# Performance work log

Hardware: AMD Instinct MI355X
Metric: run time of the kernel (lower is better)

Reference implementation:

```python
import jax, jax.numpy as jnp
import numpy as np
from jax import lax

N_USERS, N_ITEMS = 40000, 60000
N = N_USERS + N_ITEMS
D = 64
E = 800000
L = 2
BIAS = 1e-4
AUTO_T = 1.0


def setup_inputs() -> dict:
    key = jax.random.key(0)
    ks = jax.random.split(key, 12)
    emb0 = jax.random.normal(ks[0], (N, D), dtype=jnp.float32) * 0.1
    h_idx = jax.random.randint(ks[1], (E,), 0, N)
    t_idx = jax.random.randint(ks[2], (E,), 0, N)
    # symmetric normalization G = D^-1/2 A D^-1/2 (values share A's sparsity)
    deg = jax.ops.segment_sum(jnp.ones((E,), jnp.float32), h_idx, num_segments=N)
    dis = jnp.where(deg > 0, deg ** -0.5, 0.0)
    G_values = dis[h_idx] * dis[t_idx]
    # Gumbel noise: -log(-log(U(bias, 1-bias)))
    ue = jax.random.uniform(ks[3], (L, E), minval=BIAS, maxval=1.0 - BIAS)
    edge_gumbel = -jnp.log(-jnp.log(ue))
    un = jax.random.uniform(ks[4], (L, N, D), minval=BIAS, maxval=1.0 - BIAS)
    emb_gumbel = -jnp.log(-jnp.log(un))
    sc2, sc1 = (2.0 / (3 * D)) ** 0.5, (2.0 / (2 * D)) ** 0.5
    edge_W1 = jax.random.normal(ks[5], (L, 2 * D, D), dtype=jnp.float32) * sc2
    edge_b1 = jnp.zeros((L, D), jnp.float32)
    edge_W2 = jax.random.normal(ks[6], (L, D, 1), dtype=jnp.float32) * sc1
    edge_b2 = jnp.zeros((L, 1), jnp.float32)
    emb_W1 = jax.random.normal(ks[7], (L, D, D), dtype=jnp.float32) * sc1
    emb_b1 = jnp.zeros((L, D), jnp.float32)
    emb_W2 = jax.random.normal(ks[8], (L, D, D), dtype=jnp.float32) * sc1
    emb_b2 = jnp.zeros((L, D), jnp.float32)
    return dict(emb0=emb0, h_idx=h_idx, t_idx=t_idx, G_values=G_values,
                edge_gumbel=edge_gumbel, emb_gumbel=emb_gumbel,
                edge_W1=edge_W1, edge_b1=edge_b1, edge_W2=edge_W2, edge_b2=edge_b2,
                emb_W1=emb_W1, emb_b1=emb_b1, emb_W2=emb_W2, emb_b2=emb_b2)


def _spmm(vals, h, t, x, n):
    # out[h] += vals * x[t]
    return jax.ops.segment_sum(vals[:, None] * x[t], h, num_segments=n)


def reference(emb0, h_idx, t_idx, G_values, edge_gumbel, emb_gumbel,
              edge_W1, edge_b1, edge_W2, edge_b2,
              emb_W1, emb_b1, emb_W2, emb_b2):
    n = emb0.shape[0]
    e0 = e1 = e2 = emb0
    s0 = s1 = s2 = emb0
    for i in range(edge_W1.shape[0]):
        # branch 0: plain normalized propagation
        gnn0 = _spmm(G_values, h_idx, t_idx, e0, n)
        # branch 1: learned edge reweighting (auto_augment_s, is_norm=True)
        edge_emb = jnp.concatenate([e1[h_idx], e1[t_idx]], axis=1)      # [E, 2D]
        logits = jnp.maximum(edge_emb @ edge_W1[i] + edge_b1[i], 0.0) @ edge_W2[i] + edge_b2[i]  # [E,1]
        w = jax.nn.sigmoid((edge_gumbel[i][:, None] + logits) / AUTO_T)[:, 0]
        w = lax.stop_gradient(w)                                         # detached in original
        row = jax.ops.segment_sum(w, h_idx, num_segments=n)
        dinv = jnp.where(row > 0, 1.0 / row, 0.0)                        # pow(-1).nan_to_num(0)
        vals1 = dinv[h_idx] * w
        gnn1 = _spmm(vals1, h_idx, t_idx, e1, n)
        # branch 2: learned feature gating (auto_augment_f)
        lg = jnp.maximum(e2 @ emb_W1[i] + emb_b1[i], 0.0) @ emb_W2[i] + emb_b2[i]
        gate = lax.stop_gradient(jax.nn.sigmoid((emb_gumbel[i] + lg) / AUTO_T))
        gnn2 = _spmm(G_values, h_idx, t_idx, gate * e2, n)
        e0 = gnn0 + e0
        e1 = gnn1 + e1
        e2 = gnn2 + e2
        s0 = s0 + e0
        s1 = s1 + e1
        s2 = s2 + e2
    return jnp.stack([s0, s1, s2])  # [3, N, D]; split rows into users/items downstream
```

## Files before the change

kernel.cpp:

```cpp
#include <hip/hip_runtime.h>
#include <hip/hip_bf16.h>
#include <math.h>

#define PK_STRIDE 256
#define LDA 72

typedef float v4f __attribute__((ext_vector_type(4)));
typedef __attribute__((ext_vector_type(8))) short s8;
typedef __attribute__((ext_vector_type(4))) float f4;

__device__ __forceinline__ float4 f4z() { return make_float4(0.f, 0.f, 0.f, 0.f); }
__device__ __forceinline__ void fma4(float4& a, float s, const float4& v) {
  a.x = fmaf(s, v.x, a.x); a.y = fmaf(s, v.y, a.y);
  a.z = fmaf(s, v.z, a.z); a.w = fmaf(s, v.w, a.w);
}
__device__ __forceinline__ float4 add4(const float4& a, const float4& b) {
  return make_float4(a.x + b.x, a.y + b.y, a.z + b.z, a.w + b.w);
}
__device__ __forceinline__ void stnt4(float* p, const float4& v) {
  v4f u; u.x = v.x; u.y = v.y; u.z = v.z; u.w = v.w;
  __builtin_nontemporal_store(u, (v4f*)p);
}
__device__ __forceinline__ float4 lo4(const uint4& u) {
  float4 f;
  f.x = __uint_as_float(u.x << 16);
  f.y = __uint_as_float(u.x & 0xffff0000u);
  f.z = __uint_as_float(u.y << 16);
  f.w = __uint_as_float(u.y & 0xffff0000u);
  return f;
}
__device__ __forceinline__ float4 hi4(const uint4& u) {
  float4 f;
  f.x = __uint_as_float(u.z << 16);
  f.y = __uint_as_float(u.z & 0xffff0000u);
  f.z = __uint_as_float(u.w << 16);
  f.w = __uint_as_float(u.w & 0xffff0000u);
  return f;
}
__device__ __forceinline__ float4 ldbf4(const unsigned short* p) {
  ushort4 u = *(const ushort4*)p;
  float4 f;
  f.x = __uint_as_float((unsigned)u.x << 16);
  f.y = __uint_as_float((unsigned)u.y << 16);
  f.z = __uint_as_float((unsigned)u.z << 16);
  f.w = __uint_as_float((unsigned)u.w << 16);
  return f;
}
__device__ __forceinline__ unsigned short f2bf(float v) {
  __hip_bfloat16 h = __float2bfloat16(v);
  return *reinterpret_cast<unsigned short*>(&h);
}
__device__ __forceinline__ unsigned pack2(float a, float b) {
  return ((unsigned)f2bf(b) << 16) | (unsigned)f2bf(a);
}
__device__ __forceinline__ void st4bf(unsigned short* p, const float4& v) {
  ushort4 u;
  u.x = f2bf(v.x); u.y = f2bf(v.y); u.z = f2bf(v.z); u.w = f2bf(v.w);
  *(ushort4*)p = u;
}
__device__ __forceinline__ float fsig(float x) {
  return __builtin_amdgcn_rcpf(1.f + __expf(-x));
}

__global__ void init_k(const float* __restrict__ emb0, unsigned short* __restrict__ pk0,
                       unsigned short* __restrict__ e2b, int N) {
  int idx = blockIdx.x * blockDim.x + threadIdx.x;
  int n = idx >> 4, q = idx & 15;
  if (n >= N) return;
  float4 v = *(const float4*)(emb0 + (size_t)n * 64 + q * 4);
  unsigned p01 = pack2(v.x, v.y), p23 = pack2(v.z, v.w);
  uint4 u = make_uint4(p01, p23, p01, p23);
  *(uint4*)(pk0 + (size_t)n * PK_STRIDE + q * 8) = u;
  st4bf(e2b + (size_t)n * 64 + q * 4, v);
}

__global__ void hist_k(const int* __restrict__ h, int* __restrict__ deg, int E) {
  int i = blockIdx.x * blockDim.x + threadIdx.x;
  if (i < E) atomicAdd(&deg[h[i]], 1);
}

__global__ void scanA_k(const int* __restrict__ deg, int* __restrict__ rp,
                        int* __restrict__ sums, int N) {
  __shared__ int s[1024];
  int i = blockIdx.x * 1024 + threadIdx.x;
  int v = (i < N) ? deg[i] : 0;
  s[threadIdx.x] = v;
  __syncthreads();
  for (int off = 1; off < 1024; off <<= 1) {
    int t = (threadIdx.x >= (unsigned)off) ? s[threadIdx.x - off] : 0;
    __syncthreads();
    s[threadIdx.x] += t;
    __syncthreads();
  }
  if (i < N) rp[i] = s[threadIdx.x] - v;
  if (threadIdx.x == 1023) sums[blockIdx.x] = s[1023];
}

__global__ void scanB_k(int* sums, int nch) {
  int lane = threadIdx.x;
  int run = 0;
  for (int base = 0; base < nch; base += 64) {
    int v = (base + lane < nch) ? sums[base + lane] : 0;
    int incl = v;
    for (int off = 1; off < 64; off <<= 1) {
      int t = __shfl_up(incl, off, 64);
      if (lane >= off) incl += t;
    }
    if (base + lane < nch) sums[base + lane] = run + (incl - v);
    run += __shfl(incl, 63, 64);
  }
}

__global__ void scanC_k(int* __restrict__ rp, int* __restrict__ cur,
                        const int* __restrict__ sums, int N, int E) {
  int i = blockIdx.x * blockDim.x + threadIdx.x;
  if (i < N) {
    int v = rp[i] + sums[i >> 10];
    rp[i] = v; cur[i] = v;
  } else if (i == N) {
    rp[N] = E;
  }
}

__global__ void fill_k(const int* __restrict__ h, const int* __restrict__ t_idx,
                       const float* __restrict__ G, const float* __restrict__ gum,
                       int* __restrict__ cur, int4* __restrict__ emeta,
                       float* __restrict__ cgum, int E, int L) {
  int i = blockIdx.x * blockDim.x + threadIdx.x;
  if (i < E) {
    int pos = atomicAdd(&cur[h[i]], 1);
    int4 em;
    em.x = t_idx[i] * PK_STRIDE;
    em.y = __float_as_int(G[i]);
    em.z = __float_as_int(gum[i]);
    em.w = (L > 1) ? __float_as_int(gum[(size_t)E + i]) : 0;
    emeta[pos] = em;
    if (L > 2)
      for (int l = 2; l < L; l++) cgum[(size_t)l * E + pos] = gum[(size_t)l * E + i];
  }
}

__global__ void wprep_k(const float* __restrict__ edge_W1,
                        const float* __restrict__ emb_W1,
                        const float* __restrict__ emb_W2,
                        unsigned short* __restrict__ wxT,
                        unsigned short* __restrict__ w1T,
                        unsigned short* __restrict__ w2T, int L) {
  const int per = 128 * 64 + 64 * 64 + 64 * 64;
  int i = blockIdx.x * blockDim.x + threadIdx.x;
  if (i >= L * per) return;
  int layer = i / per, r = i % per;
  if (r < 8192) {
    int j = r >> 6, k = r & 63;
    float v = (j < 64) ? edge_W1[((size_t)layer * 128 + k) * 64 + j]
                       : edge_W1[((size_t)layer * 128 + 64 + k) * 64 + (j - 64)];
    wxT[(size_t)layer * 8192 + j * 64 + k] = f2bf(v);
  } else if (r < 8192 + 4096) {
    int q = r - 8192; int n = q >> 6, k = q & 63;
    w1T[(size_t)layer * 4096 + n * 64 + k] =
        f2bf(emb_W1[((size_t)layer * 64 + k) * 64 + n]);
  } else {
    int q = r - 12288; int n = q >> 6, k = q & 63;
    w2T[(size_t)layer * 4096 + n * 64 + k] =
        f2bf(emb_W2[((size_t)layer * 64 + k) * 64 + n]);
  }
}

__global__ __launch_bounds__(256) void dense_k(
    const unsigned short* __restrict__ pkin,
    const unsigned short* __restrict__ e2b,
    const unsigned short* __restrict__ wxT,
    const unsigned short* __restrict__ w1T,
    const unsigned short* __restrict__ w2T,
    const float* __restrict__ b1,
    const float* __restrict__ b2,
    const float* __restrict__ gum,
    unsigned short* __restrict__ xhb,
    unsigned short* __restrict__ pk,
    int N) {
  __shared__ unsigned short a1[64 * LDA];
  __shared__ unsigned short a2[64 * LDA];
  __shared__ unsigned short wx[128 * LDA];
  __shared__ unsigned short w1[64 * LDA];
  __shared__ unsigned short w2[64 * LDA];
  int tid = threadIdx.x;
  int n0 = blockIdx.x * 64;
  for (int i = tid; i < 64 * 16; i += 256) {
    int r = i >> 4, c = i & 15;
    ushort4 v1 = make_ushort4(0, 0, 0, 0), v2 = v1;
    if (n0 + r < N) {
      v1 = *(const ushort4*)(pkin + (size_t)(n0 + r) * PK_STRIDE + c * 8 + 4);
      v2 = *(const ushort4*)(e2b + (size_t)(n0 + r) * 64 + c * 4);
    }
    *(ushort4*)(a1 + r * LDA + c * 4) = v1;
    *(ushort4*)(a2 + r * LDA + c * 4) = v2;
  }
  for (int i = tid; i < 128 * 8; i += 256) {
    int r = i >> 3, s = i & 7;
    *(uint4*)(wx + r * LDA + s * 8) = *(const uint4*)(wxT + r * 64 + s * 8);
  }
  for (int i = tid; i < 64 * 8; i += 256) {
    int r = i >> 3, s = i & 7;
    *(uint4*)(w1 + r * LDA + s * 8) = *(const uint4*)(w1T + r * 64 + s * 8);
    *(uint4*)(w2 + r * LDA + s * 8) = *(const uint4*)(w2T + r * 64 + s * 8);
  }
  __syncthreads();
  int wv = tid >> 6, l = tid & 63;
  int l15 = l & 15, lg = l >> 4;
  int wr = wv * 16;
  int arow = wr + l15;
  s8 af1_0 = *(const s8*)(a1 + arow * LDA + 8 * lg);
  s8 af1_1 = *(const s8*)(a1 + arow * LDA + 32 + 8 * lg);
#pragma unroll
  for (int ct = 0; ct < 8; ct++) {
    f4 acc = {0.f, 0.f, 0.f, 0.f};
    s8 b0 = *(const s8*)(wx + (ct * 16 + l15) * LDA + 8 * lg);
    s8 bI = *(const s8*)(wx + (ct * 16 + l15) * LDA + 32 + 8 * lg);
    acc = __builtin_amdgcn_mfma_f32_16x16x32_bf16(af1_0, b0, acc, 0, 0, 0);
    acc = __builtin_amdgcn_mfma_f32_16x16x32_bf16(af1_1, bI, acc, 0, 0, 0);
#pragma unroll
    for (int j = 0; j < 4; j++) {
      int n = n0 + wr + lg * 4 + j;
      if (n < N) {
        if (ct < 4) {
          xhb[(size_t)n * 64 + ct * 16 + l15] = f2bf(acc[j]);
        } else {
          int c2 = (ct - 4) * 16 + l15;
          pk[(size_t)n * PK_STRIDE + 128 + (c2 >> 2) * 8 + 4 + (c2 & 3)] = f2bf(acc[j]);
        }
      }
    }
  }
  s8 af2_0 = *(const s8*)(a2 + arow * LDA + 8 * lg);
  s8 af2_1 = *(const s8*)(a2 + arow * LDA + 32 + 8 * lg);
#pragma unroll
  for (int ct = 0; ct < 4; ct++) {
    f4 acc = {0.f, 0.f, 0.f, 0.f};
    s8 b0 = *(const s8*)(w1 + (ct * 16 + l15) * LDA + 8 * lg);
    s8 bI = *(const s8*)(w1 + (ct * 16 + l15) * LDA + 32 + 8 * lg);
    acc = __builtin_amdgcn_mfma_f32_16x16x32_bf16(af2_0, b0, acc, 0, 0, 0);
    acc = __builtin_amdgcn_mfma_f32_16x16x32_bf16(af2_1, bI, acc, 0, 0, 0);
    float bb = b1[ct * 16 + l15];
#pragma unroll
    for (int j = 0; j < 4; j++) {
      float h = fmaxf(acc[j] + bb, 0.f);
      a1[(wr + lg * 4 + j) * LDA + ct * 16 + l15] = f2bf(h);
    }
  }
  s8 afh_0 = *(const s8*)(a1 + arow * LDA + 8 * lg);
  s8 afh_1 = *(const s8*)(a1 + arow * LDA + 32 + 8 * lg);
#pragma unroll
  for (int ct = 0; ct < 4; ct++) {
    f4 acc = {0.f, 0.f, 0.f, 0.f};
    s8 b0 = *(const s8*)(w2 + (ct * 16 + l15) * LDA + 8 * lg);
    s8 bI = *(const s8*)(w2 + (ct * 16 + l15) * LDA + 32 + 8 * lg);
    acc = __builtin_amdgcn_mfma_f32_16x16x32_bf16(afh_0, b0, acc, 0, 0, 0);
    acc = __builtin_amdgcn_mfma_f32_16x16x32_bf16(afh_1, bI, acc, 0, 0, 0);
    int c2 = ct * 16 + l15;
    float bb = b2[c2];
#pragma unroll
    for (int j = 0; j < 4; j++) {
      int row = wr + lg * 4 + j;
      int n = n0 + row;
      if (n < N) {
        float gv = gum[(size_t)n * 64 + c2];
        float e2v = __uint_as_float((unsigned)a2[row * LDA + c2] << 16);
        float y = e2v * fsig(gv + acc[j] + bb);
        pk[(size_t)n * PK_STRIDE + 128 + (c2 >> 2) * 8 + (c2 & 3)] = f2bf(y);
      }
    }
  }
}

#define CH 2

#define LOADCH(Abuf, Bbuf, I0)                                          \
  _Pragma("unroll")                                                     \
  for (int c = 0; c < CH; c++) {                                        \
    int i_ = (I0) + c;                                                  \
    int tof_ = __shfl(em.x, i_ & 15, 16);                               \
    if (i_ < cnt) {                                                     \
      const unsigned short* pr_ = pk + (size_t)tof_ + l * 8;            \
      Abuf[c] = *(const uint4*)(pr_);                                   \
      Bbuf[c] = *(const uint4*)(pr_ + 128);                             \
    }                                                                   \
  }

#define COMPCH(Abuf, Bbuf, I0)                                          \
  _Pragma("unroll")                                                     \
  for (int c = 0; c < CH; c++) {                                        \
    int i_ = (I0) + c;                                                  \
    float gg_ = __shfl(__int_as_float(em.y), i_ & 15, 16);              \
    float gu_ = __shfl(guv, i_ & 15, 16);                               \
    if (i_ < cnt) {                                                     \
      float4 v0_ = lo4(Abuf[c]);                                        \
      float4 v1_ = hi4(Abuf[c]);                                        \
      float4 vy_ = lo4(Bbuf[c]);                                        \
      float4 xt_ = hi4(Bbuf[c]);                                        \
      float pq_ = fmaxf(xb1.x + xt_.x, 0.f) * w2v.x                     \
                + fmaxf(xb1.y + xt_.y, 0.f) * w2v.y                     \
                + fmaxf(xb1.z + xt_.z, 0.f) * w2v.z                     \
                + fmaxf(xb1.w + xt_.w, 0.f) * w2v.w;                    \
      pq_ += __shfl_xor(pq_, 1, 16);                                    \
      pq_ += __shfl_xor(pq_, 2, 16);                                    \
      pq_ += __shfl_xor(pq_, 4, 16);                                    \
      pq_ += __shfl_xor(pq_, 8, 16);                                    \
      float w_ = fsig(gu_ + pq_ + b2s);                                 \
      wsum += w_;                                                       \
      fma4(acc0, gg_, v0_);                                             \
      fma4(acc1, w_, v1_);                                              \
      fma4(acc2, gg_, vy_);                                             \
    }                                                                   \
  }

template <int FIRST, int OUTM, int GSEL>
__global__ __launch_bounds__(256) void spmm3f_k(const int* __restrict__ rp,
    const int4* __restrict__ emeta, const float* __restrict__ cgum,
    const unsigned short* __restrict__ pk, const unsigned short* __restrict__ xhb,
    const unsigned short* __restrict__ e2b_in,
    const float* __restrict__ b1, const float* __restrict__ W2,
    const float* __restrict__ b2, const float* __restrict__ emb0,
    unsigned short* __restrict__ pkn, unsigned short* __restrict__ e2b,
    float* __restrict__ out0, float* __restrict__ out1, float* __restrict__ out2,
    int N) {
  int g = threadIdx.x >> 4;
  int l = threadIdx.x & 15;
  int n = blockIdx.x * 16 + g;
  if (n >= N) return;
  int jb = rp[n], je = rp[n + 1];
  size_t o64 = (size_t)n * 64 + l * 4;
  float4 xh4 = ldbf4(xhb + o64);
  float4 b1v = *(const float4*)(b1 + l * 4);
  float4 xb1 = add4(xh4, b1v);
  float4 w2v = *(const float4*)(W2 + l * 4);
  float b2s = b2[0];
  float4 rc0, rc1, rc2;
  if (FIRST) {
    rc0 = *(const float4*)(emb0 + o64);
    rc1 = rc0; rc2 = rc0;
  } else {
    uint4 rA = *(const uint4*)(pk + (size_t)n * PK_STRIDE + l * 8);
    rc0 = lo4(rA);
    rc1 = hi4(rA);
    rc2 = ldbf4(e2b_in + o64);
  }
  float4 acc0 = f4z(), acc1 = f4z(), acc2 = f4z();
  float wsum = 0.f;
  for (int base = jb; base < je; base += 16) {
    int idx = base + l;
    bool valid = idx < je;
    int4 em = valid ? emeta[idx] : make_int4(0, 0, 0, 0);
    float guv;
    if (GSEL == 0) guv = __int_as_float(em.z);
    else if (GSEL == 1) guv = __int_as_float(em.w);
    else guv = valid ? cgum[idx] : 0.f;
    int cnt = min(16, je - base);
    uint4 A0[CH], B0[CH], A1[CH], B1[CH];
    LOADCH(A0, B0, 0)
    for (int i0 = 0; i0 < cnt; i0 += 2 * CH) {
      LOADCH(A1, B1, i0 + CH)
      COMPCH(A0, B0, i0)
      LOADCH(A0, B0, i0 + 2 * CH)
      COMPCH(A1, B1, i0 + CH)
    }
  }
  float dinv = (wsum > 0.f) ? __builtin_amdgcn_rcpf(wsum) : 0.f;
  float4 en0 = add4(acc0, rc0);
  acc1.x *= dinv; acc1.y *= dinv; acc1.z *= dinv; acc1.w *= dinv;
  float4 en1 = add4(acc1, rc1);
  float4 en2 = add4(acc2, rc2);
  if (OUTM != 1) {
    uint4 wA;
    wA.x = pack2(en0.x, en0.y); wA.y = pack2(en0.z, en0.w);
    wA.z = pack2(en1.x, en1.y); wA.w = pack2(en1.z, en1.w);
    *(uint4*)(pkn + (size_t)n * PK_STRIDE + l * 8) = wA;
    st4bf(e2b + o64, en2);
  }
  if (OUTM == 1) {
    float4 base = *(const float4*)(emb0 + o64);
    stnt4(out0 + o64, add4(base, add4(rc0, en0)));
    stnt4(out1 + o64, add4(base, add4(rc1, en1)));
    stnt4(out2 + o64, add4(base, add4(rc2, en2)));
  } else if (OUTM == 2) {
    *(float4*)(out0 + o64) = add4(rc0, en0);
    *(float4*)(out1 + o64) = add4(rc1, en1);
    *(float4*)(out2 + o64) = add4(rc2, en2);
  } else if (OUTM == 3) {
    *(float4*)(out0 + o64) = add4(*(const float4*)(out0 + o64), en0);
    *(float4*)(out1 + o64) = add4(*(const float4*)(out1 + o64), en1);
    *(float4*)(out2 + o64) = add4(*(const float4*)(out2 + o64), en2);
  }
}

extern "C" void kernel_launch(void* const* d_in, const int* in_sizes, int n_in,
                              void* d_out, int out_size, void* d_ws, size_t ws_size,
                              hipStream_t stream) {
  const float* emb0        = (const float*)d_in[0];
  const int*   h_idx       = (const int*)d_in[1];
  const int*   t_idx       = (const int*)d_in[2];
  const float* G_values    = (const float*)d_in[3];
  const float* edge_gumbel = (const float*)d_in[4];
  const float* emb_gumbel  = (const float*)d_in[5];
  const float* edge_W1     = (const float*)d_in[6];
  const float* edge_b1     = (const float*)d_in[7];
  const float* edge_W2     = (const float*)d_in[8];
  const float* edge_b2     = (const float*)d_in[9];
  const float* emb_W1      = (const float*)d_in[10];
  const float* emb_b1      = (const float*)d_in[11];
  const float* emb_W2      = (const float*)d_in[12];
  const float* emb_b2      = (const float*)d_in[13];

  const int D = 64;
  const int N = in_sizes[0] / D;
  const int E = in_sizes[1];
  const int L = in_sizes[4] / E;
  const size_t ND = (size_t)N * D;

  char* p = (char*)d_ws;
  auto alloc = [&](size_t bytes) -> char* {
    char* r = p;
    p += (bytes + 255) & ~(size_t)255;
    return r;
  };
  unsigned short* xhb = (unsigned short*)alloc(ND * 2);
  unsigned short* e2b = (unsigned short*)alloc(ND * 2);
  unsigned short* pkA = (unsigned short*)alloc((size_t)N * PK_STRIDE * 2);
  unsigned short* pkB = (unsigned short*)alloc((size_t)N * PK_STRIDE * 2);
  int4*  emeta = (int4*)alloc((size_t)E * 16);
  float* cgum  = (float*)alloc((size_t)L * E * 4);
  unsigned short* wxT = (unsigned short*)alloc((size_t)L * 8192 * 2);
  unsigned short* w1T = (unsigned short*)alloc((size_t)L * 4096 * 2);
  unsigned short* w2T = (unsigned short*)alloc((size_t)L * 4096 * 2);
  int*   deg   = (int*)alloc((size_t)N * 4);
  int*   cur   = (int*)alloc((size_t)N * 4);
  int*   rp    = (int*)alloc(((size_t)N + 1) * 4);
  int*   sums  = (int*)alloc(1024 * 4);

  float* out = (float*)d_out;

  init_k<<<(N * 16 + 255) / 256, 256, 0, stream>>>(emb0, pkA, e2b, N);
  hipMemsetAsync(deg, 0, (size_t)N * 4, stream);
  hist_k<<<(E + 255) / 256, 256, 0, stream>>>(h_idx, deg, E);
  int nch = (N + 1023) / 1024;
  scanA_k<<<nch, 1024, 0, stream>>>(deg, rp, sums, N);
  scanB_k<<<1, 64, 0, stream>>>(sums, nch);
  scanC_k<<<(N + 256) / 256, 256, 0, stream>>>(rp, cur, sums, N, E);
  fill_k<<<(E + 255) / 256, 256, 0, stream>>>(h_idx, t_idx, G_values, edge_gumbel,
                                              cur, emeta, cgum, E, L);
  wprep_k<<<(L * 16384 + 255) / 256, 256, 0, stream>>>(edge_W1, emb_W1, emb_W2,
                                                       wxT, w1T, w2T, L);

  int nb64 = (N + 63) / 64;
  int nb16 = (N + 15) / 16;

  for (int i = 0; i < L; i++) {
    unsigned short* pkc = (i & 1) ? pkB : pkA;
    unsigned short* pkn = (i & 1) ? pkA : pkB;
    dense_k<<<nb64, 256, 0, stream>>>(pkc, e2b,
                                      wxT + (size_t)i * 8192,
                                      w1T + (size_t)i * 4096,
                                      w2T + (size_t)i * 4096,
                                      emb_b1 + (size_t)i * 64,
                                      emb_b2 + (size_t)i * 64,
                                      emb_gumbel + (size_t)i * ND,
                                      xhb, pkc, N);
    const float* cg = cgum + (size_t)i * E;
    const float* eb1 = edge_b1 + (size_t)i * 64;
    const float* eW2 = edge_W2 + (size_t)i * 64;
    const float* eb2 = edge_b2 + i;
    if (L == 2) {
      if (i == 0)
        spmm3f_k<1, 0, 0><<<nb16, 256, 0, stream>>>(rp, emeta, cg, pkc, xhb, e2b,
                                                    eb1, eW2, eb2, emb0, pkn, e2b,
                                                    out, out + ND, out + 2 * ND, N);
      else
        spmm3f_k<0, 1, 1><<<nb16, 256, 0, stream>>>(rp, emeta, cg, pkc, xhb, e2b,
                                                    eb1, eW2, eb2, emb0, pkn, e2b,
                                                    out, out + ND, out + 2 * ND, N);
    } else {
      if (i == 0)
        spmm3f_k<1, 2, 2><<<nb16, 256, 0, stream>>>(rp, emeta, cg, pkc, xhb, e2b,
                                                    eb1, eW2, eb2, emb0, pkn, e2b,
                                                    out, out + ND, out + 2 * ND, N);
      else
        spmm3f_k<0, 3, 2><<<nb16, 256, 0, stream>>>(rp, emeta, cg, pkc, xhb, e2b,
                                                    eb1, eW2, eb2, emb0, pkn, e2b,
                                                    out, out + ND, out + 2 * ND, N);
    }
  }
}
```

Before: 346.3 us.

## Sort CSR edges within each row by target-index bucket for gather locality

The CSR build now buckets edges by (head row, tail index >> 13), giving about 13 buckets per row. Within each row, edges come out grouped by coarse target range. The aim is to improve cache locality of the x[t] gathers in the SpMM, since rows processed in parallel then tend to touch similar target regions at the same time. The cost is a count/scan array about 13x larger, which makes the scan and memset kernels more expensive, and gumbel selection for L>2 is reorganized.

```diff
diff --git a/kernel.cpp b/kernel.cpp
--- a/kernel.cpp
+++ b/kernel.cpp
@@ -4,6 +4,7 @@
 
 #define PK_STRIDE 256
 #define LDA 72
+#define TSHIFT 13
 
 typedef float v4f __attribute__((ext_vector_type(4)));
 typedef __attribute__((ext_vector_type(8))) short s8;
@@ -74,16 +75,17 @@
   st4bf(e2b + (size_t)n * 64 + q * 4, v);
 }
 
-__global__ void hist_k(const int* __restrict__ h, int* __restrict__ deg, int E) {
+__global__ void hist_k(const int* __restrict__ h, const int* __restrict__ t,
+                       int* __restrict__ deg, int E, int B) {
   int i = blockIdx.x * blockDim.x + threadIdx.x;
-  if (i < E) atomicAdd(&deg[h[i]], 1);
+  if (i < E) atomicAdd(&deg[(size_t)h[i] * B + ((unsigned)t[i] >> TSHIFT)], 1);
 }
 
 __global__ void scanA_k(const int* __restrict__ deg, int* __restrict__ rp,
-                        int* __restrict__ sums, int N) {
+                        int* __restrict__ sums, int NB) {
   __shared__ int s[1024];
   int i = blockIdx.x * 1024 + threadIdx.x;
-  int v = (i < N) ? deg[i] : 0;
+  int v = (i < NB) ? deg[i] : 0;
   s[threadIdx.x] = v;
   __syncthreads();
   for (int off = 1; off < 1024; off <<= 1) {
@@ -92,7 +94,7 @@
     s[threadIdx.x] += t;
     __syncthreads();
   }
-  if (i < N) rp[i] = s[threadIdx.x] - v;
+  if (i < NB) rp[i] = s[threadIdx.x] - v;
   if (threadIdx.x == 1023) sums[blockIdx.x] = s[1023];
 }
 
@@ -112,25 +114,26 @@
 }
 
 __global__ void scanC_k(int* __restrict__ rp, int* __restrict__ cur,
-                        const int* __restrict__ sums, int N, int E) {
+                        const int* __restrict__ sums, int NB, int E) {
   int i = blockIdx.x * blockDim.x + threadIdx.x;
-  if (i < N) {
+  if (i < NB) {
     int v = rp[i] + sums[i >> 10];
     rp[i] = v; cur[i] = v;
-  } else if (i == N) {
-    rp[N] = E;
+  } else if (i == NB) {
+    rp[NB] = E;
   }
 }
 
 __global__ void fill_k(const int* __restrict__ h, const int* __restrict__ t_idx,
                        const float* __restrict__ G, const float* __restrict__ gum,
                        int* __restrict__ cur, int4* __restrict__ emeta,
-                       float* __restrict__ cgum, int E, int L) {
+                       float* __restrict__ cgum, int E, int L, int B) {
   int i = blockIdx.x * blockDim.x + threadIdx.x;
   if (i < E) {
-    int pos = atomicAdd(&cur[h[i]], 1);
+    int t = t_idx[i];
+    int pos = atomicAdd(&cur[(size_t)h[i] * B + ((unsigned)t >> TSHIFT)], 1);
     int4 em;
-    em.x = t_idx[i] * PK_STRIDE;
+    em.x = t * PK_STRIDE;
     em.y = __float_as_int(G[i]);
     em.z = __float_as_int(gum[i]);
     em.w = (L > 1) ? __float_as_int(gum[(size_t)E + i]) : 0;
@@ -322,12 +325,12 @@
     const float* __restrict__ b2, const float* __restrict__ emb0,
     unsigned short* __restrict__ pkn, unsigned short* __restrict__ e2b,
     float* __restrict__ out0, float* __restrict__ out1, float* __restrict__ out2,
-    int N) {
+    int N, int B) {
   int g = threadIdx.x >> 4;
   int l = threadIdx.x & 15;
   int n = blockIdx.x * 16 + g;
   if (n >= N) return;
-  int jb = rp[n], je = rp[n + 1];
+  int jb = rp[(size_t)n * B], je = rp[(size_t)(n + 1) * B];
   size_t o64 = (size_t)n * 64 + l * 4;
   float4 xh4 = ldbf4(xhb + o64);
   float4 b1v = *(const float4*)(b1 + l * 4);
@@ -415,6 +418,8 @@
   const int E = in_sizes[1];
   const int L = in_sizes[4] / E;
   const size_t ND = (size_t)N * D;
+  const int B = (N + (1 << TSHIFT) - 1) >> TSHIFT;
+  const size_t NB = (size_t)N * B;
 
   char* p = (char*)d_ws;
   auto alloc = [&](size_t bytes) -> char* {
@@ -427,26 +432,26 @@
   unsigned short* pkA = (unsigned short*)alloc((size_t)N * PK_STRIDE * 2);
   unsigned short* pkB = (unsigned short*)alloc((size_t)N * PK_STRIDE * 2);
   int4*  emeta = (int4*)alloc((size_t)E * 16);
-  float* cgum  = (float*)alloc((size_t)L * E * 4);
+  float* cgum  = (float*)alloc((L > 2 ? (size_t)L * E : 1) * 4);
   unsigned short* wxT = (unsigned short*)alloc((size_t)L * 8192 * 2);
   unsigned short* w1T = (unsigned short*)alloc((size_t)L * 4096 * 2);
   unsigned short* w2T = (unsigned short*)alloc((size_t)L * 4096 * 2);
-  int*   deg   = (int*)alloc((size_t)N * 4);
-  int*   cur   = (int*)alloc((size_t)N * 4);
-  int*   rp    = (int*)alloc(((size_t)N + 1) * 4);
-  int*   sums  = (int*)alloc(1024 * 4);
+  int*   deg   = (int*)alloc(NB * 4);
+  int*   cur   = (int*)alloc(NB * 4);
+  int*   rp    = (int*)alloc((NB + 1) * 4);
+  int*   sums  = (int*)alloc(4096 * 4);
 
   float* out = (float*)d_out;
 
   init_k<<<(N * 16 + 255) / 256, 256, 0, stream>>>(emb0, pkA, e2b, N);
-  hipMemsetAsync(deg, 0, (size_t)N * 4, stream);
-  hist_k<<<(E + 255) / 256, 256, 0, stream>>>(h_idx, deg, E);
-  int nch = (N + 1023) / 1024;
-  scanA_k<<<nch, 1024, 0, stream>>>(deg, rp, sums, N);
+  hipMemsetAsync(deg, 0, NB * 4, stream);
+  hist_k<<<(E + 255) / 256, 256, 0, stream>>>(h_idx, t_idx, deg, E, B);
+  int nch = (int)((NB + 1023) / 1024);
+  scanA_k<<<nch, 1024, 0, stream>>>(deg, rp, sums, (int)NB);
   scanB_k<<<1, 64, 0, stream>>>(sums, nch);
-  scanC_k<<<(N + 256) / 256, 256, 0, stream>>>(rp, cur, sums, N, E);
+  scanC_k<<<(int)((NB + 256) / 256), 256, 0, stream>>>(rp, cur, sums, (int)NB, E);
   fill_k<<<(E + 255) / 256, 256, 0, stream>>>(h_idx, t_idx, G_values, edge_gumbel,
-                                              cur, emeta, cgum, E, L);
+                                              cur, emeta, cgum, E, L, B);
   wprep_k<<<(L * 16384 + 255) / 256, 256, 0, stream>>>(edge_W1, emb_W1, emb_W2,
                                                        wxT, w1T, w2T, L);
 
@@ -464,7 +469,7 @@
                                       emb_b2 + (size_t)i * 64,
                                       emb_gumbel + (size_t)i * ND,
                                       xhb, pkc, N);
-    const float* cg = cgum + (size_t)i * E;
+    const float* cg = cgum;
     const float* eb1 = edge_b1 + (size_t)i * 64;
     const float* eW2 = edge_W2 + (size_t)i * 64;
     const float* eb2 = edge_b2 + i;
@@ -472,20 +477,25 @@
       if (i == 0)
         spmm3f_k<1, 0, 0><<<nb16, 256, 0, stream>>>(rp, emeta, cg, pkc, xhb, e2b,
                                                     eb1, eW2, eb2, emb0, pkn, e2b,
-                                                    out, out + ND, out + 2 * ND, N);
+                                                    out, out + ND, out + 2 * ND, N, B);
       else
         spmm3f_k<0, 1, 1><<<nb16, 256, 0, stream>>>(rp, emeta, cg, pkc, xhb, e2b,
                                                     eb1, eW2, eb2, emb0, pkn, e2b,
-                                                    out, out + ND, out + 2 * ND, N);
+                                                    out, out + ND, out + 2 * ND, N, B);
     } else {
+      const float* cgl = cgum + (size_t)i * E;
       if (i == 0)
-        spmm3f_k<1, 2, 2><<<nb16, 256, 0, stream>>>(rp, emeta, cg, pkc, xhb, e2b,
+        spmm3f_k<1, 2, 0><<<nb16, 256, 0, stream>>>(rp, emeta, cgl, pkc, xhb, e2b,
                                                     eb1, eW2, eb2, emb0, pkn, e2b,
-                                                    out, out + ND, out + 2 * ND, N);
+                                                    out, out + ND, out + 2 * ND, N, B);
+      else if (i == 1)
+        spmm3f_k<0, 3, 1><<<nb16, 256, 0, stream>>>(rp, emeta, cgl, pkc, xhb, e2b,
+                                                    eb1, eW2, eb2, emb0, pkn, e2b,
+                                                    out, out + ND, out + 2 * ND, N, B);
       else
-        spmm3f_k<0, 3, 2><<<nb16, 256, 0, stream>>>(rp, emeta, cg, pkc, xhb, e2b,
+        spmm3f_k<0, 3, 2><<<nb16, 256, 0, stream>>>(rp, emeta, cgl, pkc, xhb, e2b,
                                                     eb1, eW2, eb2, emb0, pkn, e2b,
-                                                    out, out + ND, out + 2 * ND, N);
-    }
-  }
-}
+                                                    out, out + ND, out + 2 * ND, N, B);
+    }
+  }
+}
```

Result: slower. 363.5 us (+5.0%).

## Fold emb0 bf16 packing into first dense pass and use compact first-layer gathers

Applied to the files above, without the earlier changes.

Removes the separate init kernel and has the first-layer dense kernel convert emb0 to bf16 directly, writing a compact 64-wide bf16 copy. In layer 0 all three branches share emb0, so the sparse kernel gathers one 8-byte slice from that compact copy instead of a 16-byte packed pair, cutting gather traffic. It also shrinks the gumbel workspace when L==2. The cost is an extra workspace buffer and more template variants; it also adjusts GSEL selection for the L>2 path.

```diff
diff --git a/kernel.cpp b/kernel.cpp
--- a/kernel.cpp
+++ b/kernel.cpp
@@ -35,6 +35,14 @@
   f.y = __uint_as_float(u.z & 0xffff0000u);
   f.z = __uint_as_float(u.w << 16);
   f.w = __uint_as_float(u.w & 0xffff0000u);
+  return f;
+}
+__device__ __forceinline__ float4 cvt2(const uint2& u) {
+  float4 f;
+  f.x = __uint_as_float(u.x << 16);
+  f.y = __uint_as_float(u.x & 0xffff0000u);
+  f.z = __uint_as_float(u.y << 16);
+  f.w = __uint_as_float(u.y & 0xffff0000u);
   return f;
 }
 __device__ __forceinline__ float4 ldbf4(const unsigned short* p) {
@@ -60,18 +68,6 @@
 }
 __device__ __forceinline__ float fsig(float x) {
   return __builtin_amdgcn_rcpf(1.f + __expf(-x));
-}
-
-__global__ void init_k(const float* __restrict__ emb0, unsigned short* __restrict__ pk0,
-                       unsigned short* __restrict__ e2b, int N) {
-  int idx = blockIdx.x * blockDim.x + threadIdx.x;
-  int n = idx >> 4, q = idx & 15;
-  if (n >= N) return;
-  float4 v = *(const float4*)(emb0 + (size_t)n * 64 + q * 4);
-  unsigned p01 = pack2(v.x, v.y), p23 = pack2(v.z, v.w);
-  uint4 u = make_uint4(p01, p23, p01, p23);
-  *(uint4*)(pk0 + (size_t)n * PK_STRIDE + q * 8) = u;
-  st4bf(e2b + (size_t)n * 64 + q * 4, v);
 }
 
 __global__ void hist_k(const int* __restrict__ h, int* __restrict__ deg, int E) {
@@ -166,7 +162,9 @@
   }
 }
 
+template <int FIRST>
 __global__ __launch_bounds__(256) void dense_k(
+    const float* __restrict__ emb0,
     const unsigned short* __restrict__ pkin,
     const unsigned short* __restrict__ e2b,
     const unsigned short* __restrict__ wxT,
@@ -177,6 +175,7 @@
     const float* __restrict__ gum,
     unsigned short* __restrict__ xhb,
     unsigned short* __restrict__ pk,
+    unsigned short* __restrict__ emb0b,
     int N) {
   __shared__ unsigned short a1[64 * LDA];
   __shared__ unsigned short a2[64 * LDA];
@@ -185,15 +184,32 @@
   __shared__ unsigned short w2[64 * LDA];
   int tid = threadIdx.x;
   int n0 = blockIdx.x * 64;
-  for (int i = tid; i < 64 * 16; i += 256) {
-    int r = i >> 4, c = i & 15;
-    ushort4 v1 = make_ushort4(0, 0, 0, 0), v2 = v1;
-    if (n0 + r < N) {
-      v1 = *(const ushort4*)(pkin + (size_t)(n0 + r) * PK_STRIDE + c * 8 + 4);
-      v2 = *(const ushort4*)(e2b + (size_t)(n0 + r) * 64 + c * 4);
-    }
-    *(ushort4*)(a1 + r * LDA + c * 4) = v1;
-    *(ushort4*)(a2 + r * LDA + c * 4) = v2;
+  if (FIRST) {
+    for (int i = tid; i < 64 * 8; i += 256) {
+      int r = i >> 3, c8 = (i & 7) * 8;
+      uint4 u = make_uint4(0, 0, 0, 0);
+      if (n0 + r < N) {
+        const float* src = emb0 + (size_t)(n0 + r) * 64 + c8;
+        float4 lo = *(const float4*)src;
+        float4 hi = *(const float4*)(src + 4);
+        u.x = pack2(lo.x, lo.y); u.y = pack2(lo.z, lo.w);
+        u.z = pack2(hi.x, hi.y); u.w = pack2(hi.z, hi.w);
+        *(uint4*)(emb0b + (size_t)(n0 + r) * 64 + c8) = u;
+      }
+      *(uint4*)(a1 + r * LDA + c8) = u;
+      *(uint4*)(a2 + r * LDA + c8) = u;
+    }
+  } else {
+    for (int i = tid; i < 64 * 16; i += 256) {
+      int r = i >> 4, c = i & 15;
+      ushort4 v1 = make_ushort4(0, 0, 0, 0), v2 = v1;
+      if (n0 + r < N) {
+        v1 = *(const ushort4*)(pkin + (size_t)(n0 + r) * PK_STRIDE + c * 8 + 4);
+        v2 = *(const ushort4*)(e2b + (size_t)(n0 + r) * 64 + c * 4);
+      }
+      *(ushort4*)(a1 + r * LDA + c * 4) = v1;
+      *(ushort4*)(a2 + r * LDA + c * 4) = v2;
+    }
   }
   for (int i = tid; i < 128 * 8; i += 256) {
     int r = i >> 3, s = i & 7;
@@ -313,11 +329,49 @@
     }                                                                   \
   }
 
+#define LOADCH_F(Abuf, Bbuf, I0)                                        \
+  _Pragma("unroll")                                                     \
+  for (int c = 0; c < CH; c++) {                                        \
+    int i_ = (I0) + c;                                                  \
+    int tof_ = __shfl(em.x, i_ & 15, 16);                               \
+    if (i_ < cnt) {                                                     \
+      Abuf[c] = *(const uint2*)(emb0b + (size_t)(tof_ >> 2) + l * 4);   \
+      Bbuf[c] = *(const uint4*)(pk + (size_t)tof_ + 128 + l * 8);       \
+    }                                                                   \
+  }
+
+#define COMPCH_F(Abuf, Bbuf, I0)                                        \
+  _Pragma("unroll")                                                     \
+  for (int c = 0; c < CH; c++) {                                        \
+    int i_ = (I0) + c;                                                  \
+    float gg_ = __shfl(__int_as_float(em.y), i_ & 15, 16);              \
+    float gu_ = __shfl(guv, i_ & 15, 16);                               \
+    if (i_ < cnt) {                                                     \
+      float4 v0_ = cvt2(Abuf[c]);                                       \
+      float4 vy_ = lo4(Bbuf[c]);                                        \
+      float4 xt_ = hi4(Bbuf[c]);                                        \
+      float pq_ = fmaxf(xb1.x + xt_.x, 0.f) * w2v.x                     \
+                + fmaxf(xb1.y + xt_.y, 0.f) * w2v.y                     \
+                + fmaxf(xb1.z + xt_.z, 0.f) * w2v.z                     \
+                + fmaxf(xb1.w + xt_.w, 0.f) * w2v.w;                    \
+      pq_ += __shfl_xor(pq_, 1, 16);                                    \
+      pq_ += __shfl_xor(pq_, 2, 16);                                    \
+      pq_ += __shfl_xor(pq_, 4, 16);                                    \
+      pq_ += __shfl_xor(pq_, 8, 16);                                    \
+      float w_ = fsig(gu_ + pq_ + b2s);                                 \
+      wsum += w_;                                                       \
+      fma4(acc0, gg_, v0_);                                             \
+      fma4(acc1, w_, v0_);                                              \
+      fma4(acc2, gg_, vy_);                                             \
+    }                                                                   \
+  }
+
 template <int FIRST, int OUTM, int GSEL>
 __global__ __launch_bounds__(256) void spmm3f_k(const int* __restrict__ rp,
     const int4* __restrict__ emeta, const float* __restrict__ cgum,
     const unsigned short* __restrict__ pk, const unsigned short* __restrict__ xhb,
     const unsigned short* __restrict__ e2b_in,
+    const unsigned short* __restrict__ emb0b,
     const float* __restrict__ b1, const float* __restrict__ W2,
     const float* __restrict__ b2, const float* __restrict__ emb0,
     unsigned short* __restrict__ pkn, unsigned short* __restrict__ e2b,
@@ -355,13 +409,25 @@
     else if (GSEL == 1) guv = __int_as_float(em.w);
     else guv = valid ? cgum[idx] : 0.f;
     int cnt = min(16, je - base);
-    uint4 A0[CH], B0[CH], A1[CH], B1[CH];
-    LOADCH(A0, B0, 0)
-    for (int i0 = 0; i0 < cnt; i0 += 2 * CH) {
-      LOADCH(A1, B1, i0 + CH)
-      COMPCH(A0, B0, i0)
-      LOADCH(A0, B0, i0 + 2 * CH)
-      COMPCH(A1, B1, i0 + CH)
+    if (FIRST) {
+      uint2 A0[CH], A1[CH];
+      uint4 B0[CH], B1[CH];
+      LOADCH_F(A0, B0, 0)
+      for (int i0 = 0; i0 < cnt; i0 += 2 * CH) {
+        LOADCH_F(A1, B1, i0 + CH)
+        COMPCH_F(A0, B0, i0)
+        LOADCH_F(A0, B0, i0 + 2 * CH)
+        COMPCH_F(A1, B1, i0 + CH)
+      }
+    } else {
+      uint4 A0[CH], B0[CH], A1[CH], B1[CH];
+      LOADCH(A0, B0, 0)
+      for (int i0 = 0; i0 < cnt; i0 += 2 * CH) {
+        LOADCH(A1, B1, i0 + CH)
+        COMPCH(A0, B0, i0)
+        LOADCH(A0, B0, i0 + 2 * CH)
+        COMPCH(A1, B1, i0 + CH)
+      }
     }
   }
   float dinv = (wsum > 0.f) ? __builtin_amdgcn_rcpf(wsum) : 0.f;
@@ -422,12 +488,13 @@
     p += (bytes + 255) & ~(size_t)255;
     return r;
   };
-  unsigned short* xhb = (unsigned short*)alloc(ND * 2);
-  unsigned short* e2b = (unsigned short*)alloc(ND * 2);
-  unsigned short* pkA = (unsigned short*)alloc((size_t)N * PK_STRIDE * 2);
-  unsigned short* pkB = (unsigned short*)alloc((size_t)N * PK_STRIDE * 2);
+  unsigned short* xhb   = (unsigned short*)alloc(ND * 2);
+  unsigned short* e2b   = (unsigned short*)alloc(ND * 2);
+  unsigned short* emb0b = (unsigned short*)alloc(ND * 2);
+  unsigned short* pkA   = (unsigned short*)alloc((size_t)N * PK_STRIDE * 2);
+  unsigned short* pkB   = (unsigned short*)alloc((size_t)N * PK_STRIDE * 2);
   int4*  emeta = (int4*)alloc((size_t)E * 16);
-  float* cgum  = (float*)alloc((size_t)L * E * 4);
+  float* cgum  = (float*)alloc((L > 2 ? (size_t)L * E : 1) * 4);
   unsigned short* wxT = (unsigned short*)alloc((size_t)L * 8192 * 2);
   unsigned short* w1T = (unsigned short*)alloc((size_t)L * 4096 * 2);
   unsigned short* w2T = (unsigned short*)alloc((size_t)L * 4096 * 2);
@@ -438,7 +505,6 @@
 
   float* out = (float*)d_out;
 
-  init_k<<<(N * 16 + 255) / 256, 256, 0, stream>>>(emb0, pkA, e2b, N);
   hipMemsetAsync(deg, 0, (size_t)N * 4, stream);
   hist_k<<<(E + 255) / 256, 256, 0, stream>>>(h_idx, deg, E);
   int nch = (N + 1023) / 1024;
@@ -456,35 +522,50 @@
   for (int i = 0; i < L; i++) {
     unsigned short* pkc = (i & 1) ? pkB : pkA;
     unsigned short* pkn = (i & 1) ? pkA : pkB;
-    dense_k<<<nb64, 256, 0, stream>>>(pkc, e2b,
-                                      wxT + (size_t)i * 8192,
-                                      w1T + (size_t)i * 4096,
-                                      w2T + (size_t)i * 4096,
-                                      emb_b1 + (size_t)i * 64,
-                                      emb_b2 + (size_t)i * 64,
-                                      emb_gumbel + (size_t)i * ND,
-                                      xhb, pkc, N);
-    const float* cg = cgum + (size_t)i * E;
+    if (i == 0)
+      dense_k<1><<<nb64, 256, 0, stream>>>(emb0, pkc, e2b,
+                                           wxT, w1T, w2T,
+                                           emb_b1, emb_b2, emb_gumbel,
+                                           xhb, pkc, emb0b, N);
+    else
+      dense_k<0><<<nb64, 256, 0, stream>>>(emb0, pkc, e2b,
+                                           wxT + (size_t)i * 8192,
+                                           w1T + (size_t)i * 4096,
+                                           w2T + (size_t)i * 4096,
+                                           emb_b1 + (size_t)i * 64,
+                                           emb_b2 + (size_t)i * 64,
+                                           emb_gumbel + (size_t)i * ND,
+                                           xhb, pkc, emb0b, N);
     const float* eb1 = edge_b1 + (size_t)i * 64;
     const float* eW2 = edge_W2 + (size_t)i * 64;
     const float* eb2 = edge_b2 + i;
     if (L == 2) {
       if (i == 0)
-        spmm3f_k<1, 0, 0><<<nb16, 256, 0, stream>>>(rp, emeta, cg, pkc, xhb, e2b,
-                                                    eb1, eW2, eb2, emb0, pkn, e2b,
+        spmm3f_k<1, 0, 0><<<nb16, 256, 0, stream>>>(rp, emeta, cgum, pkc, xhb, e2b,
+                                                    emb0b, eb1, eW2, eb2, emb0,
+                                                    pkn, e2b,
                                                     out, out + ND, out + 2 * ND, N);
       else
-        spmm3f_k<0, 1, 1><<<nb16, 256, 0, stream>>>(rp, emeta, cg, pkc, xhb, e2b,
-                                                    eb1, eW2, eb2, emb0, pkn, e2b,
+        spmm3f_k<0, 1, 1><<<nb16, 256, 0, stream>>>(rp, emeta, cgum, pkc, xhb, e2b,
+                                                    emb0b, eb1, eW2, eb2, emb0,
+                                                    pkn, e2b,
                                                     out, out + ND, out + 2 * ND, N);
     } else {
+      const float* cgl = (L > 2) ? cgum + (size_t)i * E : cgum;
       if (i == 0)
-        spmm3f_k<1, 2, 2><<<nb16, 256, 0, stream>>>(rp, emeta, cg, pkc, xhb, e2b,
-                                                    eb1, eW2, eb2, emb0, pkn, e2b,
+        spmm3f_k<1, 2, 0><<<nb16, 256, 0, stream>>>(rp, emeta, cgl, pkc, xhb, e2b,
+                                                    emb0b, eb1, eW2, eb2, emb0,
+                                                    pkn, e2b,
+                                                    out, out + ND, out + 2 * ND, N);
+      else if (i == 1)
+        spmm3f_k<0, 3, 1><<<nb16, 256, 0, stream>>>(rp, emeta, cgl, pkc, xhb, e2b,
+                                                    emb0b, eb1, eW2, eb2, emb0,
+                                                    pkn, e2b,
                                                     out, out + ND, out + 2 * ND, N);
       else
-        spmm3f_k<0, 3, 2><<<nb16, 256, 0, stream>>>(rp, emeta, cg, pkc, xhb, e2b,
-                                                    eb1, eW2, eb2, emb0, pkn, e2b,
+        spmm3f_k<0, 3, 2><<<nb16, 256, 0, stream>>>(rp, emeta, cgl, pkc, xhb, e2b,
+                                                    emb0b, eb1, eW2, eb2, emb0,
+                                                    pkn, e2b,
                                                     out, out + ND, out + 2 * ND, N);
     }
   }
```

After: 331.4 us. -4.3%, faster.
